# Optimization experiments

Measured on AMD Instinct MI355X. Metric: run time of the kernel, lower is better.

Reference implementation:

```python
import jax, jax.numpy as jnp
import numpy as np

DIM = 768
HEADS = 12
HEAD_DIM = DIM // HEADS
WS = 14  # window size
MLP = 3072
EPS = 1e-6
SCALE = HEAD_DIM ** -0.5
B, H, W = 4, 64, 64


def setup_inputs() -> dict:
    key = jax.random.key(0)
    ks = jax.random.split(key, 8)
    s = 0.02
    f32 = jnp.float32
    return {
        "hidden_states": jax.random.normal(ks[0], (B, DIM, H, W), f32),
        "ln1_w": jnp.ones((DIM,), f32),
        "ln1_b": jnp.zeros((DIM,), f32),
        "qkv_w": jax.random.normal(ks[1], (DIM, 3 * DIM), f32) * s,
        "qkv_b": jnp.zeros((3 * DIM,), f32),
        "proj_w": jax.random.normal(ks[2], (DIM, DIM), f32) * s,
        "proj_b": jnp.zeros((DIM,), f32),
        "rel_pos_h": jax.random.normal(ks[3], (2 * WS - 1, HEAD_DIM), f32) * s,
        "rel_pos_w": jax.random.normal(ks[4], (2 * WS - 1, HEAD_DIM), f32) * s,
        "ln2_w": jnp.ones((DIM,), f32),
        "ln2_b": jnp.zeros((DIM,), f32),
        "fc1_w": jax.random.normal(ks[5], (DIM, MLP), f32) * s,
        "fc1_b": jnp.zeros((MLP,), f32),
        "fc2_w": jax.random.normal(ks[6], (MLP, DIM), f32) * s,
        "fc2_b": jnp.zeros((DIM,), f32),
    }


def _layer_norm(x, w, b):
    mu = jnp.mean(x, axis=-1, keepdims=True)
    var = jnp.mean(jnp.square(x - mu), axis=-1, keepdims=True)
    return (x - mu) * jax.lax.rsqrt(var + EPS) * w + b


def _get_rel_pos(size, rel_pos):
    # q_size == k_size == WS, rel_pos already has 2*WS-1 rows -> pure gather
    coords = jnp.arange(size)[:, None] - jnp.arange(size)[None, :] + (size - 1)
    return rel_pos[coords]  # (size, size, head_dim)


def _attention(x, qkv_w, qkv_b, proj_w, proj_b, rel_pos_h, rel_pos_w):
    nb, h, w, c = x.shape  # windows batch, WS, WS, DIM
    n = h * w
    qkv = x.reshape(nb, n, c) @ qkv_w + qkv_b  # (nb, n, 3*DIM)
    qkv = qkv.reshape(nb, n, 3, HEADS, HEAD_DIM).transpose(2, 0, 3, 1, 4)
    qkv = qkv.reshape(3, nb * HEADS, n, HEAD_DIM)
    q, k, v = qkv[0], qkv[1], qkv[2]
    attn = jnp.einsum('bqc,bkc->bqk', q * SCALE, k)  # (nb*HEADS, n, n)
    # decomposed relative position bias
    Rh = _get_rel_pos(h, rel_pos_h)  # (h, h, hd)
    Rw = _get_rel_pos(w, rel_pos_w)  # (w, w, hd)
    rq = q.reshape(-1, h, w, HEAD_DIM)
    rel_h = jnp.einsum('bhwc,hkc->bhwk', rq, Rh)
    rel_w = jnp.einsum('bhwc,wkc->bhwk', rq, Rw)
    attn = (attn.reshape(-1, h, w, h, w)
            + rel_h[:, :, :, :, None]
            + rel_w[:, :, :, None, :]).reshape(-1, n, n)
    attn = jax.nn.softmax(attn, axis=-1)
    out = attn @ v  # (nb*HEADS, n, hd)
    out = out.reshape(nb, HEADS, h, w, HEAD_DIM).transpose(0, 2, 3, 1, 4)
    out = out.reshape(nb, h, w, c)
    return out @ proj_w + proj_b


def reference(hidden_states, ln1_w, ln1_b, qkv_w, qkv_b, proj_w, proj_b,
              rel_pos_h, rel_pos_w, ln2_w, ln2_b, fc1_w, fc1_b, fc2_w, fc2_b):
    x = hidden_states.transpose(0, 2, 3, 1)  # NCHW -> NHWC
    b, h, w, c = x.shape
    shortcut = x
    x = _layer_norm(x, ln1_w, ln1_b)
    # window partition with padding
    ph = (WS - h % WS) % WS
    pw = (WS - w % WS) % WS
    x = jnp.pad(x, ((0, 0), (0, ph), (0, pw), (0, 0)))
    hp, wp = h + ph, w + pw
    x = x.reshape(b, hp // WS, WS, wp // WS, WS, c).transpose(0, 1, 3, 2, 4, 5)
    windows = x.reshape(-1, WS, WS, c)
    windows = _attention(windows, qkv_w, qkv_b, proj_w, proj_b, rel_pos_h, rel_pos_w)
    # window unpartition + crop
    x = windows.reshape(b, hp // WS, wp // WS, WS, WS, c).transpose(0, 1, 3, 2, 4, 5)
    x = x.reshape(b, hp, wp, c)[:, :h, :w, :]
    x = shortcut + x
    y = _layer_norm(x, ln2_w, ln2_b)
    y = jax.nn.gelu(y @ fc1_w + fc1_b, approximate=False) @ fc2_w + fc2_b
    x = x + y
    return x.transpose(0, 3, 1, 2)  # back to NCHW
```

## Files before the change

kernel.cpp:

```cpp
#include <hip/hip_runtime.h>
#include <cstdint>
#include <cstddef>

#define NIMG   4
#define GRIDSZ 64
#define CH     768
#define NHEAD  12
#define WSZ    14
#define NWINS  100
#define NTOK   196
#define MWIN   19600
#define MREAL  16384
#define MLPC   3072
#define QKSCALE 0.125f

#define KSTR 72
#define VSTR 216
#define PSTR 40

typedef unsigned short u16;
typedef __attribute__((ext_vector_type(8))) short bf16x8;
typedef __attribute__((ext_vector_type(4))) float f32x4;

__device__ __forceinline__ float b2f(u16 u) {
  uint32_t x = (uint32_t)u << 16; float f; __builtin_memcpy(&f, &x, 4); return f;
}
__device__ __forceinline__ u16 f2b(float f) {
  uint32_t x; __builtin_memcpy(&x, &f, 4);
  x += 0x7fffu + ((x >> 16) & 1u);
  return (u16)(x >> 16);
}

__device__ __forceinline__ float fast_gelu(float x) {
  float z  = x * 0.70710678118654752440f;
  float az = fabsf(z);
  float t  = 1.0f / (1.0f + 0.3275911f * az);
  float poly = ((((1.061405429f * t - 1.453152027f) * t + 1.421413741f) * t
                 - 0.284496736f) * t + 0.254829592f) * t;
  float e  = __expf(-az * az);
  float erfv = copysignf(1.0f - poly * e, z);
  return 0.5f * x * (1.0f + erfv);
}

__device__ __forceinline__ void gl_lds16(const u16* g, u16* l) {
  __builtin_amdgcn_global_load_lds(
      (const __attribute__((address_space(1))) unsigned int*)g,
      (__attribute__((address_space(3))) unsigned int*)l, 16, 0, 0);
}

__global__ __launch_bounds__(256) void k_nchw2nhwc(const float* __restrict__ in,
                                                   float* __restrict__ out) {
  __shared__ float tile[32][33];
  int b  = blockIdx.z;
  int g0 = blockIdx.x * 32;
  int c0 = blockIdx.y * 32;
  int tx = threadIdx.x, ty = threadIdx.y;
  const float* ip = in + (size_t)b * CH * 4096;
  float* op = out + (size_t)b * 4096 * CH;
#pragma unroll
  for (int k = 0; k < 32; k += 8)
    tile[ty + k][tx] = ip[(size_t)(c0 + ty + k) * 4096 + g0 + tx];
  __syncthreads();
#pragma unroll
  for (int k = 0; k < 32; k += 8)
    op[(size_t)(g0 + ty + k) * CH + c0 + tx] = tile[tx][ty + k];
}

__global__ __launch_bounds__(256) void k_nhwc2nchw(const float* __restrict__ in,
                                                   float* __restrict__ out) {
  __shared__ float tile[32][33];
  int b  = blockIdx.z;
  int g0 = blockIdx.x * 32;
  int c0 = blockIdx.y * 32;
  int tx = threadIdx.x, ty = threadIdx.y;
  const float* ip = in + (size_t)b * 4096 * CH;
  float* op = out + (size_t)b * CH * 4096;
#pragma unroll
  for (int k = 0; k < 32; k += 8)
    tile[ty + k][tx] = ip[(size_t)(g0 + ty + k) * CH + c0 + tx];
  __syncthreads();
#pragma unroll
  for (int k = 0; k < 32; k += 8)
    op[(size_t)(c0 + ty + k) * 4096 + g0 + tx] = tile[tx][ty + k];
}

__global__ __launch_bounds__(256) void k_wt(const float* __restrict__ in,
                                            u16* __restrict__ out,
                                            int K, int N) {
  __shared__ float t[32][33];
  int n0 = blockIdx.x * 32, k0 = blockIdx.y * 32;
  int tx = threadIdx.x, ty = threadIdx.y;
#pragma unroll
  for (int k = 0; k < 32; k += 8)
    t[ty + k][tx] = in[(size_t)(k0 + ty + k) * N + n0 + tx];
  __syncthreads();
#pragma unroll
  for (int k = 0; k < 32; k += 8)
    out[(size_t)(n0 + ty + k) * K + k0 + tx] = f2b(t[tx][ty + k]);
}

__device__ __forceinline__ float block_sum(float s, float* red) {
  __syncthreads();
#pragma unroll
  for (int off = 32; off > 0; off >>= 1) s += __shfl_down(s, off, 64);
  int wid = threadIdx.x >> 6, lane = threadIdx.x & 63;
  if (lane == 0) red[wid] = s;
  __syncthreads();
  return red[0] + red[1] + red[2] + red[3];
}

__global__ __launch_bounds__(256) void k_ln(const float* __restrict__ x,
                                            const float* __restrict__ wt,
                                            const float* __restrict__ bs,
                                            u16* __restrict__ y,
                                            int window_mode) {
  __shared__ float red[4];
  int row = blockIdx.x, tid = threadIdx.x;
  const float* xp = x + (size_t)row * CH;
  float v0 = xp[tid], v1 = xp[tid + 256], v2 = xp[tid + 512];
  float mu = block_sum(v0 + v1 + v2, red) * (1.0f / 768.0f);
  float d0 = v0 - mu, d1 = v1 - mu, d2 = v2 - mu;
  float var = block_sum(d0 * d0 + d1 * d1 + d2 * d2, red) * (1.0f / 768.0f);
  float rs = rsqrtf(var + 1e-6f);
  int orow = row;
  if (window_mode) {
    int b = row >> 12, hw = row & 4095;
    int h = hw >> 6, wc = hw & 63;
    orow = (b * 25 + (h / WSZ) * 5 + (wc / WSZ)) * NTOK + (h % WSZ) * WSZ + (wc % WSZ);
  }
  u16* yp = y + (size_t)orow * CH;
  yp[tid]       = f2b(d0 * rs * wt[tid]       + bs[tid]);
  yp[tid + 256] = f2b(d1 * rs * wt[tid + 256] + bs[tid + 256]);
  yp[tid + 512] = f2b(d2 * rs * wt[tid + 512] + bs[tid + 512]);
}

__global__ __launch_bounds__(256) void k_gemm_mfma(const u16* __restrict__ A,
                                                   const u16* __restrict__ BT,
                                                   const float* __restrict__ bias,
                                                   void* __restrict__ Cv,
                                                   u16* __restrict__ Vt,
                                                   int M, int N, int K,
                                                   int act, int mode, int row0) {
  __shared__ u16 As[2][128 * 32];
  __shared__ u16 Bs[2][128 * 32];
  int tid  = threadIdx.x;
  int lane = tid & 63, wave = tid >> 6;

  int gx   = gridDim.x;
  int nwg  = gx * gridDim.y;
  int orig = blockIdx.y * gx + blockIdx.x;
  int q = nwg >> 3, r = nwg & 7;
  int xcd = orig & 7, idx = orig >> 3;
  int wgid = (xcd < r ? xcd * (q + 1) : r * (q + 1) + (xcd - r) * q) + idx;
  int bn = wgid % gx, bm = wgid / gx;

  int wm = (wave & 1) * 64, wn = (wave >> 1) * 64;
  int l15 = lane & 15, quad = lane >> 4;

  f32x4 acc[4][4];
#pragma unroll
  for (int i = 0; i < 4; i++)
#pragma unroll
    for (int j = 0; j < 4; j++) acc[i][j] = (f32x4){0.f, 0.f, 0.f, 0.f};

  const u16* Atile = A + (size_t)bm * 128 * K;
  const u16* Btile = BT + (size_t)bn * 128 * K;

  int c0 = wave * 64 + lane;
  int c1 = c0 + 256;
  int ar0 = c0 >> 2, ao0 = (c0 & 3) * 8;
  int ar1 = c1 >> 2, ao1 = (c1 & 3) * 8;
  int lo0 = (wave * 64) * 8;
  int lo1 = (256 + wave * 64) * 8;

  const int nk = K >> 5;

  gl_lds16(Atile + (size_t)ar0 * K + ao0, &As[0][lo0]);
  gl_lds16(Atile + (size_t)ar1 * K + ao1, &As[0][lo1]);
  gl_lds16(Btile + (size_t)ar0 * K + ao0, &Bs[0][lo0]);
  gl_lds16(Btile + (size_t)ar1 * K + ao1, &Bs[0][lo1]);
  __syncthreads();

  for (int t = 0; t < nk; ++t) {
    int cur = t & 1;
    if (t + 1 < nk) {
      int kk = (t + 1) << 5;
      gl_lds16(Atile + (size_t)ar0 * K + kk + ao0, &As[cur ^ 1][lo0]);
      gl_lds16(Atile + (size_t)ar1 * K + kk + ao1, &As[cur ^ 1][lo1]);
      gl_lds16(Btile + (size_t)ar0 * K + kk + ao0, &Bs[cur ^ 1][lo0]);
      gl_lds16(Btile + (size_t)ar1 * K + kk + ao1, &Bs[cur ^ 1][lo1]);
    }
    bf16x8 af[4], bfv[4];
#pragma unroll
    for (int mi = 0; mi < 4; mi++)
      af[mi] = *(const bf16x8*)&As[cur][(size_t)(wm + mi * 16 + l15) * 32 + quad * 8];
#pragma unroll
    for (int ni = 0; ni < 4; ni++)
      bfv[ni] = *(const bf16x8*)&Bs[cur][(size_t)(wn + ni * 16 + l15) * 32 + quad * 8];
#pragma unroll
    for (int mi = 0; mi < 4; mi++)
#pragma unroll
      for (int ni = 0; ni < 4; ni++)
        acc[mi][ni] = __builtin_amdgcn_mfma_f32_16x16x32_bf16(
            bfv[ni], af[mi], acc[mi][ni], 0, 0, 0);
    __syncthreads();
  }

#pragma unroll
  for (int mi = 0; mi < 4; mi++) {
    int row = bm * 128 + wm + mi * 16 + l15;
    if (row >= M) continue;
    size_t gbase = 0;
    bool valid = true;
    int wloc = 0, tok = 0;
    if (mode == 2) {
      int rowa = row + row0;
      int widx = rowa / NTOK, tt = rowa % NTOK;
      int b = widx / 25, wq = widx % 25;
      int h = (wq / 5) * WSZ + tt / WSZ;
      int w = (wq % 5) * WSZ + tt % WSZ;
      valid = (h < GRIDSZ) && (w < GRIDSZ);
      gbase = valid ? ((size_t)((b * GRIDSZ + h) * GRIDSZ + w)) * CH : 0;
    }
    if (mode == 3) { wloc = row / NTOK; tok = row - wloc * NTOK; }
#pragma unroll
    for (int ni = 0; ni < 4; ni++) {
      int colb = bn * 128 + wn + ni * 16 + quad * 4;
      float4 b4 = *(const float4*)&bias[colb];
      float v[4] = {acc[mi][ni][0] + b4.x, acc[mi][ni][1] + b4.y,
                    acc[mi][ni][2] + b4.z, acc[mi][ni][3] + b4.w};
      if (act == 1) {
#pragma unroll
        for (int r2 = 0; r2 < 4; r2++) v[r2] = fast_gelu(v[r2]);
      }
      if (mode == 0) {
        ushort4 st = make_ushort4(f2b(v[0]), f2b(v[1]), f2b(v[2]), f2b(v[3]));
        *(ushort4*)((u16*)Cv + (size_t)row * N + colb) = st;
      } else if (mode == 1) {
        float4* p = (float4*)((float*)Cv + (size_t)row * N + colb);
        float4 o = *p;
        o.x += v[0]; o.y += v[1]; o.z += v[2]; o.w += v[3];
        *p = o;
      } else if (mode == 2) {
        if (valid) {
          float4* p = (float4*)((float*)Cv + gbase + colb);
          float4 o = *p;
          o.x += v[0]; o.y += v[1]; o.z += v[2]; o.w += v[3];
          *p = o;
        }
      } else {
        if (colb < 1536) {
          ushort4 st = make_ushort4(f2b(v[0]), f2b(v[1]), f2b(v[2]), f2b(v[3]));
          *(ushort4*)((u16*)Cv + (size_t)row * N + colb) = st;
        } else {
          int vv = colb - 1536, hd = vv >> 6, d = vv & 63;
          u16* vp = Vt + ((size_t)(wloc * NHEAD + hd) * 64 + d) * VSTR + tok;
#pragma unroll
          for (int r2 = 0; r2 < 4; r2++) vp[(size_t)r2 * VSTR] = f2b(v[r2]);
        }
      }
    }
  }
}

__global__ __launch_bounds__(256) void k_relbias(const u16* __restrict__ qkv,
                                                 const float* __restrict__ rel_h,
                                                 const float* __restrict__ rel_w,
                                                 u16* __restrict__ rhg,
                                                 u16* __restrict__ rwg,
                                                 int nrows) {
  int idx = blockIdx.x * 256 + threadIdx.x;
  if (idx >= nrows * NHEAD) return;
  int head = idx % NHEAD, row = idx / NHEAD;
  int wloc = row / NTOK, tok = row - wloc * NTOK;
  const u16* qp = qkv + (size_t)row * (3 * CH) + head * 64;
  float q[64];
#pragma unroll
  for (int d = 0; d < 64; d += 4) {
    ushort4 u4 = *(const ushort4*)(qp + d);
    q[d] = b2f(u4.x); q[d + 1] = b2f(u4.y); q[d + 2] = b2f(u4.z); q[d + 3] = b2f(u4.w);
  }
  int hq = tok / WSZ, wq = tok % WSZ;
  size_t obase = ((size_t)(wloc * NHEAD + head) * NTOK + tok) * 16;
  for (int kk = 0; kk < WSZ; kk++) {
    const float* rh = rel_h + (size_t)(hq - kk + WSZ - 1) * 64;
    const float* rw = rel_w + (size_t)(wq - kk + WSZ - 1) * 64;
    float sh = 0.0f, sw = 0.0f;
#pragma unroll
    for (int d = 0; d < 64; d++) { sh += q[d] * rh[d]; sw += q[d] * rw[d]; }
    rhg[obase + kk] = f2b(sh);
    rwg[obase + kk] = f2b(sw);
  }
}

__global__ __launch_bounds__(256) void k_attn_mfma(const u16* __restrict__ qkv,
                                                   const u16* __restrict__ Vt,
                                                   const u16* __restrict__ rhg,
                                                   const u16* __restrict__ rwg,
                                                   u16* __restrict__ out,
                                                   int win0) {
  __shared__ u16 Ks[NTOK * KSTR];
  __shared__ u16 Vs[64 * VSTR];
  __shared__ u16 Ps[4][16 * PSTR];
  int head = blockIdx.x, wloc = blockIdx.y;
  int tid = threadIdx.x, lane = tid & 63, wave = tid >> 6;
  int l15 = lane & 15, quad = lane >> 4;
  const u16* qbase = qkv + (size_t)wloc * NTOK * (3 * CH) + head * 64;

  for (int c = tid; c < NTOK * 8; c += 256) {
    int tok = c >> 3, part = c & 7;
    uint4 v = *(const uint4*)(qbase + (size_t)tok * (3 * CH) + CH + part * 8);
    *(uint4*)&Ks[tok * KSTR + part * 8] = v;
  }
  const u16* vb = Vt + (size_t)(wloc * NHEAD + head) * 64 * VSTR;
#pragma unroll
  for (int it = 0; it < 7; ++it) {
    int c = it * 256 + tid;
    if (c < 64 * VSTR / 8) gl_lds16(vb + (size_t)c * 8, Vs + ((size_t)it * 256 + wave * 64) * 8);
  }
  __syncthreads();

  const u16* rhp = rhg + ((size_t)(wloc * NHEAD + head) * NTOK) * 16;
  const u16* rwp = rwg + ((size_t)(wloc * NHEAD + head) * NTOK) * 16;
  int winabs = win0 + wloc;

  for (int t16 = wave; t16 < 13; t16 += 4) {
    int qtok = t16 * 16 + l15; if (qtok > NTOK - 1) qtok = NTOK - 1;
    bf16x8 aq0 = *(const bf16x8*)(qbase + (size_t)qtok * (3 * CH) + quad * 8);
    bf16x8 aq1 = *(const bf16x8*)(qbase + (size_t)qtok * (3 * CH) + 32 + quad * 8);

    f32x4 s[13];
#pragma unroll
    for (int ct = 0; ct < 13; ct++) s[ct] = (f32x4){0.f, 0.f, 0.f, 0.f};
#pragma unroll
    for (int ct = 0; ct < 13; ct++) {
      int ktok = ct * 16 + l15; if (ktok > NTOK - 1) ktok = NTOK - 1;
      bf16x8 bk0 = *(const bf16x8*)&Ks[ktok * KSTR + quad * 8];
      bf16x8 bk1 = *(const bf16x8*)&Ks[ktok * KSTR + 32 + quad * 8];
      s[ct] = __builtin_amdgcn_mfma_f32_16x16x32_bf16(aq0, bk0, s[ct], 0, 0, 0);
      s[ct] = __builtin_amdgcn_mfma_f32_16x16x32_bf16(aq1, bk1, s[ct], 0, 0, 0);
    }

    f32x4 o[4];
#pragma unroll
    for (int ni = 0; ni < 4; ni++) o[ni] = (f32x4){0.f, 0.f, 0.f, 0.f};
    float lsum[4] = {0.f, 0.f, 0.f, 0.f};
    int row0t = t16 * 16 + quad * 4;

#pragma unroll
    for (int cc = 0; cc < 7; ++cc) {
#pragma unroll
      for (int half = 0; half < 2; ++half) {
        int ct = cc * 2 + half;
        if (ct < 13) {
          int col = ct * 16 + l15;
          int jh = col / WSZ, jw = col - jh * WSZ;
          bool colok = col < NTOK;
#pragma unroll
          for (int r = 0; r < 4; r++) {
            int rowt = row0t + r; int rowc = rowt > NTOK - 1 ? NTOK - 1 : rowt;
            float bias = b2f(rhp[rowc * 16 + jh]) + b2f(rwp[rowc * 16 + jw]);
            float sv = s[ct][r] * QKSCALE + bias;
            float p = colok ? __expf(sv) : 0.f;
            lsum[r] += p;
            Ps[wave][(quad * 4 + r) * PSTR + half * 16 + l15] = f2b(p);
          }
        } else {
#pragma unroll
          for (int r = 0; r < 4; r++)
            Ps[wave][(quad * 4 + r) * PSTR + half * 16 + l15] = 0;
        }
      }
      bf16x8 pa = *(const bf16x8*)&Ps[wave][l15 * PSTR + quad * 8];
#pragma unroll
      for (int ni = 0; ni < 4; ni++) {
        bf16x8 bv = *(const bf16x8*)&Vs[(ni * 16 + l15) * VSTR + cc * 32 + quad * 8];
        o[ni] = __builtin_amdgcn_mfma_f32_16x16x32_bf16(pa, bv, o[ni], 0, 0, 0);
      }
    }

#pragma unroll
    for (int r = 0; r < 4; r++) {
#pragma unroll
      for (int m = 1; m < 16; m <<= 1) lsum[r] += __shfl_xor(lsum[r], m, 64);
    }

#pragma unroll
    for (int r = 0; r < 4; r++) {
      int rowt = row0t + r;
      if (rowt < NTOK) {
        float inv = 1.0f / lsum[r];
        u16* op = out + ((size_t)winabs * NTOK + rowt) * CH + head * 64;
#pragma unroll
        for (int ni = 0; ni < 4; ni++) op[ni * 16 + l15] = f2b(o[ni][r] * inv);
      }
    }
  }
}

extern "C" void kernel_launch(void* const* d_in, const int* in_sizes, int n_in,
                              void* d_out, int out_size, void* d_ws, size_t ws_size,
                              hipStream_t stream) {
  const float* hidden = (const float*)d_in[0];
  const float* ln1_w  = (const float*)d_in[1];
  const float* ln1_b  = (const float*)d_in[2];
  const float* qkv_w  = (const float*)d_in[3];
  const float* qkv_b  = (const float*)d_in[4];
  const float* proj_w = (const float*)d_in[5];
  const float* proj_b = (const float*)d_in[6];
  const float* rel_h  = (const float*)d_in[7];
  const float* rel_w  = (const float*)d_in[8];
  const float* ln2_w  = (const float*)d_in[9];
  const float* ln2_b  = (const float*)d_in[10];
  const float* fc1_w  = (const float*)d_in[11];
  const float* fc1_b  = (const float*)d_in[12];
  const float* fc2_w  = (const float*)d_in[13];
  const float* fc2_b  = (const float*)d_in[14];
  float* out = (float*)d_out;

  char* ws = (char*)d_ws;
  float* x_nhwc = (float*)ws;
  u16*   R1     = (u16*)(ws + 50331648);
  u16*   qkvT   = (u16*)(ws + 80437248);
  u16*   projT  = qkvT + (size_t)2304 * 768;
  u16*   fc1T   = projT + (size_t)768 * 768;
  u16*   fc2T   = fc1T + (size_t)3072 * 768;
  u16*   R2     = fc2T + (size_t)768 * 3072;
  size_t used   = (size_t)80437248 + 14155776;
  size_t r2e    = ws_size > used ? (ws_size - used) >> 1 : 0;

  const size_t PW_QKV = (size_t)NTOK * 3 * CH;
  const size_t PW_VT  = (size_t)NHEAD * 64 * VSTR;
  const size_t PW_RB  = (size_t)NHEAD * NTOK * 16;
  const size_t perwin = PW_QKV + PW_VT + 2 * PW_RB;
  size_t wc_s = r2e / perwin;
  int Wc = wc_s >= NWINS ? NWINS : (int)wc_s;
  if (Wc < 1) Wc = 1;
  size_t rc_s = (r2e / MLPC / 128) * 128;
  int Rc = rc_s >= MREAL ? MREAL : (int)rc_s;
  if (Rc < 128) Rc = 128;

  u16* Vt  = R2 + (size_t)Wc * PW_QKV;
  u16* rhg = Vt + (size_t)Wc * PW_VT;
  u16* rwg = rhg + (size_t)Wc * PW_RB;

  k_wt<<<dim3(72, 24), dim3(32, 8), 0, stream>>>(qkv_w, qkvT, CH, 3 * CH);
  k_wt<<<dim3(24, 24), dim3(32, 8), 0, stream>>>(proj_w, projT, CH, CH);
  k_wt<<<dim3(96, 24), dim3(32, 8), 0, stream>>>(fc1_w, fc1T, CH, MLPC);
  k_wt<<<dim3(24, 96), dim3(32, 8), 0, stream>>>(fc2_w, fc2T, MLPC, CH);

  hipMemsetAsync(R1, 0, (size_t)MWIN * CH * sizeof(u16), stream);

  k_nchw2nhwc<<<dim3(128, 24, NIMG), dim3(32, 8), 0, stream>>>(hidden, x_nhwc);
  k_ln<<<MREAL, 256, 0, stream>>>(x_nhwc, ln1_w, ln1_b, R1, 1);
  for (int w0 = 0; w0 < NWINS; w0 += Wc) {
    int wc = NWINS - w0 < Wc ? NWINS - w0 : Wc;
    int Mc = wc * NTOK;
    k_gemm_mfma<<<dim3(18, (Mc + 127) / 128), 256, 0, stream>>>(
        R1 + (size_t)w0 * NTOK * CH, qkvT, qkv_b, R2, Vt,
        Mc, 3 * CH, CH, 0, 3, 0);
    k_relbias<<<(Mc * NHEAD + 255) / 256, 256, 0, stream>>>(
        R2, rel_h, rel_w, rhg, rwg, Mc);
    k_attn_mfma<<<dim3(NHEAD, wc), 256, 0, stream>>>(
        R2, Vt, rhg, rwg, R1, w0);
  }
  k_gemm_mfma<<<dim3(6, (MWIN + 127) / 128), 256, 0, stream>>>(
      R1, projT, proj_b, x_nhwc, nullptr, MWIN, CH, CH, 0, 2, 0);
  k_ln<<<MREAL, 256, 0, stream>>>(x_nhwc, ln2_w, ln2_b, R1, 0);
  for (int r0 = 0; r0 < MREAL; r0 += Rc) {
    int rc = MREAL - r0 < Rc ? MREAL - r0 : Rc;
    k_gemm_mfma<<<dim3(24, (rc + 127) / 128), 256, 0, stream>>>(
        R1 + (size_t)r0 * CH, fc1T, fc1_b, R2, nullptr, rc, MLPC, CH, 1, 0, 0);
    k_gemm_mfma<<<dim3(6, (rc + 127) / 128), 256, 0, stream>>>(
        R2, fc2T, fc2_b, x_nhwc + (size_t)r0 * CH, nullptr, rc, CH, MLPC, 0, 1, 0);
  }
  k_nhwc2nchw<<<dim3(128, 24, NIMG), dim3(32, 8), 0, stream>>>(x_nhwc, out);
}
```

Baseline: 753.7 us.

## Triple-buffer GEMM LDS staging with vmcnt-based waits and single barrier

Moves the MFMA GEMM main loop from double buffering to a three-slot LDS ring, prefetching two K-slabs ahead. Each iteration waits with a partial vmcnt instead of a full drain and uses one barrier instead of one after compute. The goal is to hide global-to-LDS latency and cut barrier stalls. It raises LDS use from 32KB to 48KB per block, which may lower occupancy, and correctness depends on the vmcnt count matching the four outstanding loads.

```diff
diff --git a/kernel.cpp b/kernel.cpp
--- a/kernel.cpp
+++ b/kernel.cpp
@@ -141,8 +141,8 @@
                                                    u16* __restrict__ Vt,
                                                    int M, int N, int K,
                                                    int act, int mode, int row0) {
-  __shared__ u16 As[2][128 * 32];
-  __shared__ u16 Bs[2][128 * 32];
+  __shared__ u16 As[3][128 * 32];
+  __shared__ u16 Bs[3][128 * 32];
   int tid  = threadIdx.x;
   int lane = tid & 63, wave = tid >> 6;
 
@@ -175,36 +175,52 @@
 
   const int nk = K >> 5;
 
-  gl_lds16(Atile + (size_t)ar0 * K + ao0, &As[0][lo0]);
-  gl_lds16(Atile + (size_t)ar1 * K + ao1, &As[0][lo1]);
-  gl_lds16(Btile + (size_t)ar0 * K + ao0, &Bs[0][lo0]);
-  gl_lds16(Btile + (size_t)ar1 * K + ao1, &Bs[0][lo1]);
-  __syncthreads();
-
-  for (int t = 0; t < nk; ++t) {
-    int cur = t & 1;
-    if (t + 1 < nk) {
-      int kk = (t + 1) << 5;
-      gl_lds16(Atile + (size_t)ar0 * K + kk + ao0, &As[cur ^ 1][lo0]);
-      gl_lds16(Atile + (size_t)ar1 * K + kk + ao1, &As[cur ^ 1][lo1]);
-      gl_lds16(Btile + (size_t)ar0 * K + kk + ao0, &Bs[cur ^ 1][lo0]);
-      gl_lds16(Btile + (size_t)ar1 * K + kk + ao1, &Bs[cur ^ 1][lo1]);
-    }
-    bf16x8 af[4], bfv[4];
-#pragma unroll
-    for (int mi = 0; mi < 4; mi++)
-      af[mi] = *(const bf16x8*)&As[cur][(size_t)(wm + mi * 16 + l15) * 32 + quad * 8];
-#pragma unroll
-    for (int ni = 0; ni < 4; ni++)
-      bfv[ni] = *(const bf16x8*)&Bs[cur][(size_t)(wn + ni * 16 + l15) * 32 + quad * 8];
-#pragma unroll
-    for (int mi = 0; mi < 4; mi++)
-#pragma unroll
-      for (int ni = 0; ni < 4; ni++)
-        acc[mi][ni] = __builtin_amdgcn_mfma_f32_16x16x32_bf16(
-            bfv[ni], af[mi], acc[mi][ni], 0, 0, 0);
-    __syncthreads();
-  }
+#define STAGE_SLAB(slot, slab)                                          \
+  do {                                                                  \
+    int kk_ = (slab) << 5;                                              \
+    gl_lds16(Atile + (size_t)ar0 * K + kk_ + ao0, &As[(slot)][lo0]);    \
+    gl_lds16(Atile + (size_t)ar1 * K + kk_ + ao1, &As[(slot)][lo1]);    \
+    gl_lds16(Btile + (size_t)ar0 * K + kk_ + ao0, &Bs[(slot)][lo0]);    \
+    gl_lds16(Btile + (size_t)ar1 * K + kk_ + ao1, &Bs[(slot)][lo1]);    \
+  } while (0)
+
+#define COMPUTE_SLAB(slot)                                                   \
+  do {                                                                       \
+    bf16x8 af[4], bfv[4];                                                    \
+    _Pragma("unroll")                                                        \
+    for (int mi = 0; mi < 4; mi++)                                           \
+      af[mi] = *(const bf16x8*)&As[(slot)][(size_t)(wm + mi * 16 + l15) * 32 \
+                                           + quad * 8];                      \
+    _Pragma("unroll")                                                        \
+    for (int ni = 0; ni < 4; ni++)                                           \
+      bfv[ni] = *(const bf16x8*)&Bs[(slot)][(size_t)(wn + ni * 16 + l15) * 32\
+                                            + quad * 8];                     \
+    _Pragma("unroll")                                                        \
+    for (int mi = 0; mi < 4; mi++)                                           \
+      _Pragma("unroll")                                                      \
+      for (int ni = 0; ni < 4; ni++)                                         \
+        acc[mi][ni] = __builtin_amdgcn_mfma_f32_16x16x32_bf16(               \
+            bfv[ni], af[mi], acc[mi][ni], 0, 0, 0);                          \
+  } while (0)
+
+  STAGE_SLAB(0, 0);
+  STAGE_SLAB(1, 1);
+
+  int t = 0;
+  for (; t < nk - 1; ++t) {
+    asm volatile("s_waitcnt vmcnt(4)" ::: "memory");
+    __builtin_amdgcn_s_barrier();
+    __builtin_amdgcn_sched_barrier(0);
+    if (t + 2 < nk) STAGE_SLAB((t + 2) % 3, t + 2);
+    COMPUTE_SLAB(t % 3);
+  }
+  asm volatile("s_waitcnt vmcnt(0)" ::: "memory");
+  __builtin_amdgcn_s_barrier();
+  __builtin_amdgcn_sched_barrier(0);
+  COMPUTE_SLAB(t % 3);
+
+#undef STAGE_SLAB
+#undef COMPUTE_SLAB
 
 #pragma unroll
   for (int mi = 0; mi < 4; mi++) {
```

Measured after the change: 758.0 us. Within noise of the previous version (+0.6%).
